# Performance work log

Hardware: AMD Instinct MI355X
Metric: run time of the kernel (lower is better)

Reference implementation:

```python
import jax, jax.numpy as jnp
import numpy as np
import math

B, S, H, NH = 8, 1024, 768, 12
DH = H // NH  # 64
EPS = 1e-5


def layernorm(x, gamma, beta):
    mu = jnp.mean(x, axis=-1, keepdims=True)
    var = jnp.mean(jnp.square(x - mu), axis=-1, keepdims=True)
    return (x - mu) * jax.lax.rsqrt(var + EPS) * gamma + beta


def setup_inputs() -> dict:
    key = jax.random.key(0)
    ks = jax.random.split(key, 12)
    sc = 1.0 / math.sqrt(H)
    return {
        "x1": jax.random.normal(ks[0], (B, S, H), jnp.float32),
        "weight_mask": jax.random.uniform(ks[1], (B, 1, S, S), jnp.float32),
        "Wq": jax.random.normal(ks[2], (H, H), jnp.float32) * sc,
        "bq": jnp.zeros((H,), jnp.float32),
        "Wk": jax.random.normal(ks[3], (H, H), jnp.float32) * sc,
        "bk": jnp.zeros((H,), jnp.float32),
        "Wv": jax.random.normal(ks[4], (H, H), jnp.float32) * sc,
        "bv": jnp.zeros((H,), jnp.float32),
        "g1": jnp.ones((H,), jnp.float32),
        "be1": jnp.zeros((H,), jnp.float32),
        "g2": jnp.ones((H,), jnp.float32),
        "be2": jnp.zeros((H,), jnp.float32),
        "W1": jax.random.normal(ks[5], (H, 2 * H), jnp.float32) * sc,
        "b1": jnp.zeros((2 * H,), jnp.float32),
        "W2": jax.random.normal(ks[6], (2 * H, H), jnp.float32) * (1.0 / math.sqrt(2 * H)),
        "b2": jnp.zeros((H,), jnp.float32),
    }


def reference(x1, weight_mask, Wq, bq, Wk, bk, Wv, bv, g1, be1, g2, be2, W1, b1, W2, b2):
    # QKV projections [B,S,H]
    q_mixed = x1 @ Wq + bq
    k_mixed = x1 @ Wk + bk
    v_mixed = x1 @ Wv + bv

    def heads(t):  # [B,S,H] -> [B,NH,S,DH]
        return t.reshape(B, S, NH, DH).transpose(0, 2, 1, 3)

    q, k, v = heads(q_mixed), heads(k_mixed), heads(v_mixed)
    scores = jnp.einsum("bhqd,bhkd->bhqk", q, k) / math.sqrt(DH)
    probs = jax.nn.softmax(scores, axis=-1)
    probs = probs * weight_mask  # post-softmax elementwise mask
    ctx = jnp.einsum("bhqk,bhkd->bhqd", probs, v)
    ctx = ctx.transpose(0, 2, 1, 3).reshape(B, S, H)

    # residual uses the mixed query (as in the original code); dropout = eval identity
    x = layernorm(ctx + q_mixed, g1, be1)
    ff = jnp.maximum(x @ W1 + b1, 0.0) @ W2 + b2
    out = layernorm(x + ff, g2, be2)
    return out
```

## Files before the change

kernel.cpp:

```cpp
#include <hip/hip_runtime.h>
#include <math.h>

#define Bsz 8
#define Sq  1024
#define Hd  768
#define NHd 12
#define DHd 64
#define QS  2304

typedef __attribute__((ext_vector_type(8))) short bf16x8;
typedef __attribute__((ext_vector_type(4))) short bf16x4;
typedef __attribute__((ext_vector_type(4))) float f32x4;
typedef __attribute__((ext_vector_type(16))) float f32x16;

__device__ __forceinline__ ushort f2bf(float f) {
    unsigned u = __float_as_uint(f);
    u += 0x7fffu + ((u >> 16) & 1u);
    return (ushort)(u >> 16);
}
__device__ __forceinline__ float bf2f(ushort u) {
    return __uint_as_float(((unsigned)u) << 16);
}
__device__ __forceinline__ void load_lds16(const ushort* g, ushort* l) {
    __builtin_amdgcn_global_load_lds((const __attribute__((address_space(1))) void*)g,
                                     (__attribute__((address_space(3))) void*)l, 16, 0, 0);
}

__device__ __forceinline__ f32x16 mfma32x8(bf16x4 a, bf16x4 b, f32x16 c) {
#if __has_builtin(__builtin_amdgcn_mfma_f32_32x32x8bf16_1k)
    return __builtin_amdgcn_mfma_f32_32x32x8bf16_1k(a, b, c, 0, 0, 0);
#elif __has_builtin(__builtin_amdgcn_mfma_f32_32x32x8_bf16)
    return __builtin_amdgcn_mfma_f32_32x32x8_bf16(a, b, c, 0, 0, 0);
#else
    bf16x8 a8 = {a[0], a[1], a[2], a[3], 0, 0, 0, 0};
    bf16x8 b8 = {b[0], b[1], b[2], b[3], 0, 0, 0, 0};
    return __builtin_amdgcn_mfma_f32_32x32x16_bf16(a8, b8, c, 0, 0, 0);
#endif
}

__global__ __launch_bounds__(256) void cvt_bf16(const float* __restrict__ a,
                                                ushort* __restrict__ o, int n4) {
    int i = blockIdx.x * 256 + threadIdx.x;
    if (i < n4) {
        float4 f = ((const float4*)a)[i];
        ushort4 u;
        u.x = f2bf(f.x); u.y = f2bf(f.y); u.z = f2bf(f.z); u.w = f2bf(f.w);
        ((ushort4*)o)[i] = u;
    }
}

__global__ __launch_bounds__(256) void transpose_cvt(const float* __restrict__ in,
                                                     ushort* __restrict__ out,
                                                     int K, int N, float scale) {
    __shared__ float tile[32][33];
    const int n0 = blockIdx.x * 32, k0 = blockIdx.y * 32;
    const int tx = threadIdx.x & 31, ty = threadIdx.x >> 5;
#pragma unroll
    for (int i = ty; i < 32; i += 8)
        tile[i][tx] = in[(size_t)(k0 + i) * N + n0 + tx] * scale;
    __syncthreads();
#pragma unroll
    for (int i = ty; i < 32; i += 8)
        out[(size_t)(n0 + i) * K + k0 + tx] = f2bf(tile[tx][i]);
}

#define KSCALE 0.18033688f

__global__ __launch_bounds__(256) void concat_bias(const float* __restrict__ bq,
                                                   const float* __restrict__ bk,
                                                   const float* __restrict__ bv,
                                                   float* __restrict__ o) {
    int i = blockIdx.x * 256 + threadIdx.x;
    if (i < 2304)
        o[i] = i < 768 ? bq[i] : (i < 1536 ? bk[i - 768] * KSCALE : bv[i - 1536]);
}

template<bool RELU, bool OUT_BF16>
__global__ __launch_bounds__(256) void gemm_mfma(const ushort* __restrict__ A,
                                                 const ushort* __restrict__ BT,
                                                 const float* __restrict__ bias,
                                                 void* __restrict__ Cout,
                                                 int M, int N, int K) {
    const int bm = blockIdx.y * 128;
    const int bn = blockIdx.x * 128;
    const int t  = threadIdx.x;
    const int wave = t >> 6, lane = t & 63;
    const int l15 = lane & 15, quad = lane >> 4;
    const int wm = (wave >> 1) * 64, wn = (wave & 1) * 64;

    __shared__ ushort As[128 * 64];
    __shared__ ushort Bs[128 * 64];

    f32x4 acc[4][4];
#pragma unroll
    for (int i = 0; i < 4; ++i)
#pragma unroll
        for (int j = 0; j < 4; ++j) acc[i][j] = (f32x4){0, 0, 0, 0};

    const int g_row[4] = {(0 * 256 + t) >> 3, (1 * 256 + t) >> 3, (2 * 256 + t) >> 3, (3 * 256 + t) >> 3};
    const int g_pc     = t & 7;

    for (int k0 = 0; k0 < K; k0 += 64) {
#pragma unroll
        for (int it = 0; it < 4; ++it) {
            const int row = g_row[it];
            const int cb  = g_pc ^ (row & 7);
            load_lds16(A  + (size_t)(bm + row) * K + k0 + cb * 8,
                       As + (size_t)(it * 256 + wave * 64) * 8);
            load_lds16(BT + (size_t)(bn + row) * K + k0 + cb * 8,
                       Bs + (size_t)(it * 256 + wave * 64) * 8);
        }
        __syncthreads();
#pragma unroll
        for (int kk = 0; kk < 64; kk += 32) {
            bf16x8 af[4], bfr[4];
            const int cbk = (kk >> 3) + quad;
#pragma unroll
            for (int i = 0; i < 4; ++i) {
                const int rowA = wm + i * 16 + l15;
                af[i]  = *(const bf16x8*)(As + (size_t)(rowA * 8 + (cbk ^ (rowA & 7))) * 8);
                const int rowB = wn + i * 16 + l15;
                bfr[i] = *(const bf16x8*)(Bs + (size_t)(rowB * 8 + (cbk ^ (rowB & 7))) * 8);
            }
#pragma unroll
            for (int i = 0; i < 4; ++i)
#pragma unroll
                for (int j = 0; j < 4; ++j)
                    acc[i][j] = __builtin_amdgcn_mfma_f32_16x16x32_bf16(af[i], bfr[j], acc[i][j], 0, 0, 0);
        }
        __syncthreads();
    }

#pragma unroll
    for (int i = 0; i < 4; ++i) {
#pragma unroll
        for (int r = 0; r < 4; ++r) {
            const int m = bm + wm + i * 16 + quad * 4 + r;
#pragma unroll
            for (int j = 0; j < 4; ++j) {
                const int n = bn + wn + j * 16 + l15;
                float v = acc[i][j][r] + bias[n];
                if (RELU) v = fmaxf(v, 0.0f);
                if (OUT_BF16) ((ushort*)Cout)[(size_t)m * N + n] = f2bf(v);
                else          ((float*)Cout)[(size_t)m * N + n] = v;
            }
        }
    }
}

__global__ __launch_bounds__(256) void v_transpose(const ushort* __restrict__ qkv,
                                                   ushort* __restrict__ vT) {
    const int bh = blockIdx.x >> 4;
    const int st = blockIdx.x & 15;
    const int b  = bh / NHd, h = bh % NHd;
    const int t  = threadIdx.x;
    __shared__ ushort T[64][72];
    {
        const int sl = t >> 2, c = (t & 3) * 16;
        const ushort* src = qkv + ((size_t)b * Sq + st * 64 + sl) * QS + 1536 + h * 64 + c;
        *(int4*)&T[sl][c]     = *(const int4*)src;
        *(int4*)&T[sl][c + 8] = *(const int4*)(src + 8);
    }
    __syncthreads();
    {
        const int d = t >> 2, kc = (t & 3) * 16;
        ushort tmp[16];
#pragma unroll
        for (int i = 0; i < 16; ++i) tmp[i] = T[kc + i][d];
        ushort* dst = vT + ((size_t)bh * 64 + d) * Sq + st * 64 + kc;
        *(int4*)dst       = *(const int4*)&tmp[0];
        *(int4*)(dst + 8) = *(const int4*)&tmp[8];
    }
}

__global__ __launch_bounds__(256, 3) void attn_mfma(const ushort* __restrict__ qkv,
                                                    const ushort* __restrict__ vT,
                                                    const ushort* __restrict__ maskb,
                                                    float* __restrict__ ctx) {
    const int nqt = Sq / 128;
    const int bh  = blockIdx.x / nqt;
    const int qt  = blockIdx.x % nqt;
    const int b   = bh / NHd;
    const int h   = bh % NHd;
    const int t   = threadIdx.x;
    const int wave = t >> 6, lane = t & 63;
    const int l31 = lane & 31, H = lane >> 5;

    __shared__ ushort Ks[2][64 * 64];
    __shared__ ushort Vs[2][64 * 64];

    const size_t rowbase = (size_t)b * Sq;
    const int q0 = qt * 128 + wave * 32;

    bf16x8 qf[4];
    {
        const ushort* qrow = qkv + (rowbase + q0 + l31) * QS + h * DHd + H * 8;
#pragma unroll
        for (int ds = 0; ds < 4; ++ds) qf[ds] = *(const bf16x8*)(qrow + ds * 16);
    }

    const int s_row[2] = {t >> 3, (256 + t) >> 3};
    const int s_pc     = t & 7;

#define STAGE(k0_, buf_)                                                            \
    {                                                                               \
        _Pragma("unroll")                                                           \
        for (int it = 0; it < 2; ++it) {                                            \
            const int row  = s_row[it];                                             \
            const int gcol = s_pc ^ (row & 7);                                      \
            load_lds16(qkv + (rowbase + (k0_) + row) * QS + Hd + h * DHd + gcol * 8,\
                       &Ks[buf_][(it * 256 + t) * 8]);                              \
            load_lds16(vT + ((size_t)bh * 64 + row) * Sq + (k0_) + gcol * 8,        \
                       &Vs[buf_][(it * 256 + t) * 8]);                              \
        }                                                                           \
    }

    STAGE(0, 0);
    __syncthreads();

    f32x16 o0, o1;
#pragma unroll
    for (int r = 0; r < 16; ++r) { o0[r] = 0.0f; o1[r] = 0.0f; }
    float rsum = 0.0f;

    const ushort* mrow = maskb + ((size_t)b * Sq + q0 + l31) * Sq;

    for (int kt = 0; kt < 16; ++kt) {
        const int k0  = kt * 64;
        const int cur = kt & 1;

        if (kt < 15) STAGE(k0 + 64, cur ^ 1);

        ushort4 mload[8];
#pragma unroll
        for (int tile = 0; tile < 2; ++tile)
#pragma unroll
            for (int rr = 0; rr < 4; ++rr)
                mload[tile * 4 + rr] = *(const ushort4*)(mrow + k0 + tile * 32 + rr * 8 + H * 4);

        f32x16 s0, s1;
#pragma unroll
        for (int r = 0; r < 16; ++r) { s0[r] = 0.0f; s1[r] = 0.0f; }
#pragma unroll
        for (int ds = 0; ds < 4; ++ds) {
            const int gk = H + 2 * ds;
            bf16x8 ka = *(const bf16x8*)&Ks[cur][(l31 * 8 + (gk ^ (l31 & 7))) * 8];
            bf16x8 kb = *(const bf16x8*)&Ks[cur][((32 + l31) * 8 + (gk ^ (l31 & 7))) * 8];
            s0 = __builtin_amdgcn_mfma_f32_32x32x16_bf16(ka, qf[ds], s0, 0, 0, 0);
            s1 = __builtin_amdgcn_mfma_f32_32x32x16_bf16(kb, qf[ds], s1, 0, 0, 0);
        }

        bf16x4 pf[8];
#pragma unroll
        for (int rr = 0; rr < 4; ++rr) {
#pragma unroll
            for (int j = 0; j < 4; ++j) {
                const float e0 = exp2f(s0[4 * rr + j]);
                const float e1 = exp2f(s1[4 * rr + j]);
                rsum += e0 + e1;
                pf[rr][j]     = (short)f2bf(e0 * bf2f(((const ushort*)&mload[rr])[j]));
                pf[4 + rr][j] = (short)f2bf(e1 * bf2f(((const ushort*)&mload[4 + rr])[j]));
            }
        }

#pragma unroll
        for (int ks = 0; ks < 8; ++ks) {
            const int sw = ks ^ (l31 & 7);
            bf16x4 va = *(const bf16x4*)&Vs[cur][(l31 * 8 + sw) * 8 + H * 4];
            bf16x4 vb = *(const bf16x4*)&Vs[cur][((32 + l31) * 8 + sw) * 8 + H * 4];
            o0 = mfma32x8(pf[ks], va, o0);
            o1 = mfma32x8(pf[ks], vb, o1);
        }
        __syncthreads();
    }

    rsum += __shfl_xor(rsum, 32);

#pragma unroll
    for (int r = 0; r < 16; ++r) {
        const int ql  = (r & 3) + 8 * (r >> 2) + 4 * H;
        const float inv = 1.0f / __shfl(rsum, ql);
        const size_t row = rowbase + q0 + ql;
        ctx[row * Hd + h * DHd + l31]      = o0[r] * inv;
        ctx[row * Hd + h * DHd + 32 + l31] = o1[r] * inv;
    }
}

template<bool RES_BF16, bool EMIT_BF16>
__global__ __launch_bounds__(256) void ln_fused(const float* __restrict__ a,
                                                const void* __restrict__ res, int res_stride,
                                                const float* __restrict__ g,
                                                const float* __restrict__ be,
                                                float* __restrict__ outf,
                                                ushort* __restrict__ outb) {
    const int row = blockIdx.x;
    const int t   = threadIdx.x;
    const float* pa = a + (size_t)row * Hd;
    __shared__ float red[4];
    float v[3];
#pragma unroll
    for (int i = 0; i < 3; ++i) {
        const int idx = t + i * 256;
        float rv;
        if (RES_BF16) rv = bf2f(((const ushort*)res)[(size_t)row * res_stride + idx]);
        else          rv = ((const float*)res)[(size_t)row * res_stride + idx];
        v[i] = pa[idx] + rv;
    }

    float s = v[0] + v[1] + v[2];
#pragma unroll
    for (int off = 32; off > 0; off >>= 1) s += __shfl_xor(s, off);
    if ((t & 63) == 0) red[t >> 6] = s;
    __syncthreads();
    const float mu = (red[0] + red[1] + red[2] + red[3]) * (1.0f / Hd);
    __syncthreads();

    float sq = 0.0f;
#pragma unroll
    for (int i = 0; i < 3; ++i) {
        v[i] -= mu;
        sq = fmaf(v[i], v[i], sq);
    }
#pragma unroll
    for (int off = 32; off > 0; off >>= 1) sq += __shfl_xor(sq, off);
    if ((t & 63) == 0) red[t >> 6] = sq;
    __syncthreads();
    const float var = (red[0] + red[1] + red[2] + red[3]) * (1.0f / Hd);
    const float rsq = rsqrtf(var + 1e-5f);
#pragma unroll
    for (int i = 0; i < 3; ++i) {
        const int idx = t + i * 256;
        const float o = v[i] * rsq * g[idx] + be[idx];
        outf[(size_t)row * Hd + idx] = o;
        if (EMIT_BF16) outb[(size_t)row * Hd + idx] = f2bf(o);
    }
}

extern "C" void kernel_launch(void* const* d_in, const int* in_sizes, int n_in,
                              void* d_out, int out_size, void* d_ws, size_t ws_size,
                              hipStream_t stream) {
    const float* x1    = (const float*)d_in[0];
    const float* wmask = (const float*)d_in[1];
    const float* Wq    = (const float*)d_in[2];
    const float* bq    = (const float*)d_in[3];
    const float* Wk    = (const float*)d_in[4];
    const float* bk    = (const float*)d_in[5];
    const float* Wv    = (const float*)d_in[6];
    const float* bv    = (const float*)d_in[7];
    const float* g1    = (const float*)d_in[8];
    const float* be1   = (const float*)d_in[9];
    const float* g2    = (const float*)d_in[10];
    const float* be2   = (const float*)d_in[11];
    const float* W1    = (const float*)d_in[12];
    const float* b1    = (const float*)d_in[13];
    const float* W2    = (const float*)d_in[14];
    const float* b2    = (const float*)d_in[15];
    float* out = (float*)d_out;

    const size_t NT = (size_t)Bsz * Sq * Hd;
    const size_t NM = (size_t)Bsz * Sq * Sq;
    const int M = Bsz * Sq;

    char* p = (char*)d_ws;
    ushort* xb     = (ushort*)p;  p += NT * 2;
    ushort* WqkvT  = (ushort*)p;  p += (size_t)2304 * 768 * 2;
    ushort* W1T    = (ushort*)p;  p += (size_t)1536 * 768 * 2;
    ushort* W2T    = (ushort*)p;  p += (size_t)768 * 1536 * 2;
    float*  qkvbias= (float*)p;   p += 2304 * 4 + 256;
    ushort* qkvb   = (ushort*)p;  p += (size_t)M * QS * 2;
    ushort* maskb  = (ushort*)p;  p += NM * 2;
    ushort* vT     = (ushort*)p;  p += (size_t)Bsz * NHd * DHd * Sq * 2;
    float*  ctxb   = (float*)p;   p += NT * 4;
    float*  xf     = (float*)p;   p += NT * 4;
    ushort* xbf    = (ushort*)p;  p += NT * 2;
    ushort* hb     = qkvb;
    float*  ffb    = ctxb;

    dim3 blk(256);

    cvt_bf16<<<dim3((int)(NT / 4 / 256)), blk, 0, stream>>>(x1, xb, (int)(NT / 4));
    cvt_bf16<<<dim3((int)(NM / 4 / 256)), blk, 0, stream>>>(wmask, maskb, (int)(NM / 4));

    transpose_cvt<<<dim3(24, 24), blk, 0, stream>>>(Wq, WqkvT,                 768, 768, 1.0f);
    transpose_cvt<<<dim3(24, 24), blk, 0, stream>>>(Wk, WqkvT + 768 * 768,     768, 768, KSCALE);
    transpose_cvt<<<dim3(24, 24), blk, 0, stream>>>(Wv, WqkvT + 2 * 768 * 768, 768, 768, 1.0f);
    transpose_cvt<<<dim3(48, 24), blk, 0, stream>>>(W1, W1T, 768, 1536, 1.0f);
    transpose_cvt<<<dim3(24, 48), blk, 0, stream>>>(W2, W2T, 1536, 768, 1.0f);
    concat_bias<<<dim3(9), blk, 0, stream>>>(bq, bk, bv, qkvbias);

    gemm_mfma<false, true><<<dim3(2304 / 128, M / 128), blk, 0, stream>>>(
        xb, WqkvT, qkvbias, qkvb, M, 2304, 768);

    v_transpose<<<dim3(Bsz * NHd * 16), blk, 0, stream>>>(qkvb, vT);

    attn_mfma<<<dim3(Bsz * NHd * (Sq / 128)), blk, 0, stream>>>(qkvb, vT, maskb, ctxb);

    ln_fused<true, true><<<dim3(M), blk, 0, stream>>>(ctxb, qkvb, QS, g1, be1, xf, xbf);

    gemm_mfma<true, true><<<dim3(1536 / 128, M / 128), blk, 0, stream>>>(
        xbf, W1T, b1, hb, M, 1536, 768);

    gemm_mfma<false, false><<<dim3(768 / 128, M / 128), blk, 0, stream>>>(
        hb, W2T, b2, ffb, M, 768, 1536);

    ln_fused<false, false><<<dim3(M), blk, 0, stream>>>(xf, ffb, Hd, g2, be2, out, nullptr);
}
```

Baseline: 384.9 us.

## Merge prep kernels, fuse V transpose into QKV GEMM, shrink W2 GEMM tile

Nine separate conversion, transpose and bias-concat launches become one multi-role prep kernel. The standalone V transpose kernel is removed: the QKV GEMM now writes the V columns straight into the transposed vT layout as packed ushort4 stores. The GEMM is templated on its M tile, and the W2 GEMM uses 64-row tiles to launch more blocks. The attention probability conversion now truncates to bf16 instead of rounding, which trades a little accuracy for fewer instructions.

```diff
diff --git a/kernel.cpp b/kernel.cpp
--- a/kernel.cpp
+++ b/kernel.cpp
@@ -38,92 +38,126 @@
 #endif
 }
 
-__global__ __launch_bounds__(256) void cvt_bf16(const float* __restrict__ a,
-                                                ushort* __restrict__ o, int n4) {
-    int i = blockIdx.x * 256 + threadIdx.x;
-    if (i < n4) {
-        float4 f = ((const float4*)a)[i];
-        ushort4 u;
-        u.x = f2bf(f.x); u.y = f2bf(f.y); u.z = f2bf(f.z); u.w = f2bf(f.w);
-        ((ushort4*)o)[i] = u;
-    }
-}
-
-__global__ __launch_bounds__(256) void transpose_cvt(const float* __restrict__ in,
-                                                     ushort* __restrict__ out,
-                                                     int K, int N, float scale) {
-    __shared__ float tile[32][33];
-    const int n0 = blockIdx.x * 32, k0 = blockIdx.y * 32;
-    const int tx = threadIdx.x & 31, ty = threadIdx.x >> 5;
-#pragma unroll
-    for (int i = ty; i < 32; i += 8)
-        tile[i][tx] = in[(size_t)(k0 + i) * N + n0 + tx] * scale;
-    __syncthreads();
-#pragma unroll
-    for (int i = ty; i < 32; i += 8)
-        out[(size_t)(n0 + i) * K + k0 + tx] = f2bf(tile[tx][i]);
-}
-
 #define KSCALE 0.18033688f
 
-__global__ __launch_bounds__(256) void concat_bias(const float* __restrict__ bq,
-                                                   const float* __restrict__ bk,
-                                                   const float* __restrict__ bv,
-                                                   float* __restrict__ o) {
-    int i = blockIdx.x * 256 + threadIdx.x;
-    if (i < 2304)
-        o[i] = i < 768 ? bq[i] : (i < 1536 ? bk[i - 768] * KSCALE : bv[i - 1536]);
-}
-
-template<bool RELU, bool OUT_BF16>
+__global__ __launch_bounds__(256) void prep(const float* __restrict__ x1,
+                                            const float* __restrict__ wmask,
+                                            const float* __restrict__ Wq,
+                                            const float* __restrict__ Wk,
+                                            const float* __restrict__ Wv,
+                                            const float* __restrict__ W1,
+                                            const float* __restrict__ W2,
+                                            const float* __restrict__ bq,
+                                            const float* __restrict__ bk,
+                                            const float* __restrict__ bv,
+                                            ushort* __restrict__ xb,
+                                            ushort* __restrict__ maskb,
+                                            ushort* __restrict__ WqkvT,
+                                            ushort* __restrict__ W1T,
+                                            ushort* __restrict__ W2T,
+                                            float* __restrict__ qkvbias) {
+    const int blk = blockIdx.x;
+    const int t   = threadIdx.x;
+    __shared__ float tl[32][33];
+
+    if (blk < 4032) {
+        const float* in; ushort* out; int Kd, Nd, ntx, tile; float sc;
+        if (blk < 1728) {
+            const int w = blk / 576; tile = blk % 576;
+            in  = (w == 0) ? Wq : (w == 1) ? Wk : Wv;
+            out = WqkvT + (size_t)w * 768 * 768;
+            Kd = 768; Nd = 768; ntx = 24;
+            sc = (w == 1) ? KSCALE : 1.0f;
+        } else if (blk < 2880) {
+            tile = blk - 1728; in = W1; out = W1T; Kd = 768; Nd = 1536; ntx = 48; sc = 1.0f;
+        } else {
+            tile = blk - 2880; in = W2; out = W2T; Kd = 1536; Nd = 768; ntx = 24; sc = 1.0f;
+        }
+        const int n0 = (tile % ntx) * 32, k0 = (tile / ntx) * 32;
+        const int tx = t & 31, ty = t >> 5;
+#pragma unroll
+        for (int i = ty; i < 32; i += 8)
+            tl[i][tx] = in[(size_t)(k0 + i) * Nd + n0 + tx] * sc;
+        __syncthreads();
+#pragma unroll
+        for (int i = ty; i < 32; i += 8)
+            out[(size_t)(n0 + i) * Kd + k0 + tx] = f2bf(tl[tx][i]);
+    } else if (blk < 7616) {
+        const int cb = blk - 4032;
+        const float4* s4;
+        ushort4* d4;
+        if (cb < 1536) { s4 = (const float4*)x1    + (size_t)cb * 1024;           d4 = (ushort4*)xb    + (size_t)cb * 1024; }
+        else           { s4 = (const float4*)wmask + (size_t)(cb - 1536) * 1024;  d4 = (ushort4*)maskb + (size_t)(cb - 1536) * 1024; }
+#pragma unroll
+        for (int i = t; i < 1024; i += 256) {
+            const float4 f = s4[i];
+            ushort4 u;
+            u.x = f2bf(f.x); u.y = f2bf(f.y); u.z = f2bf(f.z); u.w = f2bf(f.w);
+            d4[i] = u;
+        }
+    } else {
+        for (int i = t; i < 2304; i += 256)
+            qkvbias[i] = i < 768 ? bq[i] : (i < 1536 ? bk[i - 768] * KSCALE : bv[i - 1536]);
+    }
+}
+
+template<int TM, bool RELU, bool OUT_BF16, bool WRITE_VT>
 __global__ __launch_bounds__(256) void gemm_mfma(const ushort* __restrict__ A,
                                                  const ushort* __restrict__ BT,
                                                  const float* __restrict__ bias,
                                                  void* __restrict__ Cout,
+                                                 ushort* __restrict__ vT,
                                                  int M, int N, int K) {
-    const int bm = blockIdx.y * 128;
+    const int bm = blockIdx.y * (TM * 32);
     const int bn = blockIdx.x * 128;
     const int t  = threadIdx.x;
     const int wave = t >> 6, lane = t & 63;
     const int l15 = lane & 15, quad = lane >> 4;
-    const int wm = (wave >> 1) * 64, wn = (wave & 1) * 64;
-
-    __shared__ ushort As[128 * 64];
+    const int wm = (wave >> 1) * (TM * 16), wn = (wave & 1) * 64;
+
+    __shared__ ushort As[TM * 32 * 64];
     __shared__ ushort Bs[128 * 64];
 
-    f32x4 acc[4][4];
-#pragma unroll
-    for (int i = 0; i < 4; ++i)
+    f32x4 acc[TM][4];
+#pragma unroll
+    for (int i = 0; i < TM; ++i)
 #pragma unroll
         for (int j = 0; j < 4; ++j) acc[i][j] = (f32x4){0, 0, 0, 0};
 
-    const int g_row[4] = {(0 * 256 + t) >> 3, (1 * 256 + t) >> 3, (2 * 256 + t) >> 3, (3 * 256 + t) >> 3};
-    const int g_pc     = t & 7;
+    const int g_pc = t & 7;
 
     for (int k0 = 0; k0 < K; k0 += 64) {
 #pragma unroll
+        for (int it = 0; it < TM; ++it) {
+            const int row = (it * 256 + t) >> 3;
+            const int cb  = g_pc ^ (row & 7);
+            load_lds16(A + (size_t)(bm + row) * K + k0 + cb * 8,
+                       As + (size_t)(it * 256 + wave * 64) * 8);
+        }
+#pragma unroll
         for (int it = 0; it < 4; ++it) {
-            const int row = g_row[it];
+            const int row = (it * 256 + t) >> 3;
             const int cb  = g_pc ^ (row & 7);
-            load_lds16(A  + (size_t)(bm + row) * K + k0 + cb * 8,
-                       As + (size_t)(it * 256 + wave * 64) * 8);
             load_lds16(BT + (size_t)(bn + row) * K + k0 + cb * 8,
                        Bs + (size_t)(it * 256 + wave * 64) * 8);
         }
         __syncthreads();
 #pragma unroll
         for (int kk = 0; kk < 64; kk += 32) {
-            bf16x8 af[4], bfr[4];
+            bf16x8 af[TM], bfr[4];
             const int cbk = (kk >> 3) + quad;
 #pragma unroll
-            for (int i = 0; i < 4; ++i) {
+            for (int i = 0; i < TM; ++i) {
                 const int rowA = wm + i * 16 + l15;
-                af[i]  = *(const bf16x8*)(As + (size_t)(rowA * 8 + (cbk ^ (rowA & 7))) * 8);
-                const int rowB = wn + i * 16 + l15;
-                bfr[i] = *(const bf16x8*)(Bs + (size_t)(rowB * 8 + (cbk ^ (rowB & 7))) * 8);
+                af[i] = *(const bf16x8*)(As + (size_t)(rowA * 8 + (cbk ^ (rowA & 7))) * 8);
             }
 #pragma unroll
-            for (int i = 0; i < 4; ++i)
+            for (int j = 0; j < 4; ++j) {
+                const int rowB = wn + j * 16 + l15;
+                bfr[j] = *(const bf16x8*)(Bs + (size_t)(rowB * 8 + (cbk ^ (rowB & 7))) * 8);
+            }
+#pragma unroll
+            for (int i = 0; i < TM; ++i)
 #pragma unroll
                 for (int j = 0; j < 4; ++j)
                     acc[i][j] = __builtin_amdgcn_mfma_f32_16x16x32_bf16(af[i], bfr[j], acc[i][j], 0, 0, 0);
@@ -131,45 +165,34 @@
         __syncthreads();
     }
 
-#pragma unroll
-    for (int i = 0; i < 4; ++i) {
-#pragma unroll
-        for (int r = 0; r < 4; ++r) {
-            const int m = bm + wm + i * 16 + quad * 4 + r;
-#pragma unroll
-            for (int j = 0; j < 4; ++j) {
-                const int n = bn + wn + j * 16 + l15;
+    const bool vblk = WRITE_VT && (bn >= 1536);
+#pragma unroll
+    for (int i = 0; i < TM; ++i) {
+        const int m0 = bm + wm + i * 16 + quad * 4;
+#pragma unroll
+        for (int j = 0; j < 4; ++j) {
+            const int n = bn + wn + j * 16 + l15;
+            float v4[4];
+#pragma unroll
+            for (int r = 0; r < 4; ++r) {
                 float v = acc[i][j][r] + bias[n];
                 if (RELU) v = fmaxf(v, 0.0f);
-                if (OUT_BF16) ((ushort*)Cout)[(size_t)m * N + n] = f2bf(v);
-                else          ((float*)Cout)[(size_t)m * N + n] = v;
+                v4[r] = v;
             }
-        }
-    }
-}
-
-__global__ __launch_bounds__(256) void v_transpose(const ushort* __restrict__ qkv,
-                                                   ushort* __restrict__ vT) {
-    const int bh = blockIdx.x >> 4;
-    const int st = blockIdx.x & 15;
-    const int b  = bh / NHd, h = bh % NHd;
-    const int t  = threadIdx.x;
-    __shared__ ushort T[64][72];
-    {
-        const int sl = t >> 2, c = (t & 3) * 16;
-        const ushort* src = qkv + ((size_t)b * Sq + st * 64 + sl) * QS + 1536 + h * 64 + c;
-        *(int4*)&T[sl][c]     = *(const int4*)src;
-        *(int4*)&T[sl][c + 8] = *(const int4*)(src + 8);
-    }
-    __syncthreads();
-    {
-        const int d = t >> 2, kc = (t & 3) * 16;
-        ushort tmp[16];
-#pragma unroll
-        for (int i = 0; i < 16; ++i) tmp[i] = T[kc + i][d];
-        ushort* dst = vT + ((size_t)bh * 64 + d) * Sq + st * 64 + kc;
-        *(int4*)dst       = *(const int4*)&tmp[0];
-        *(int4*)(dst + 8) = *(const int4*)&tmp[8];
+            if (vblk) {
+                const int d = n - 1536;
+                const int b = m0 >> 10, s = m0 & 1023;
+                ushort4 pk;
+                pk.x = f2bf(v4[0]); pk.y = f2bf(v4[1]); pk.z = f2bf(v4[2]); pk.w = f2bf(v4[3]);
+                *(ushort4*)(vT + ((size_t)(b * NHd + (d >> 6)) * 64 + (d & 63)) * Sq + s) = pk;
+            } else {
+#pragma unroll
+                for (int r = 0; r < 4; ++r) {
+                    if (OUT_BF16) ((ushort*)Cout)[(size_t)(m0 + r) * N + n] = f2bf(v4[r]);
+                    else          ((float*)Cout)[(size_t)(m0 + r) * N + n] = v4[r];
+                }
+            }
+        }
     }
 }
 
@@ -258,8 +281,8 @@
                 const float e0 = exp2f(s0[4 * rr + j]);
                 const float e1 = exp2f(s1[4 * rr + j]);
                 rsum += e0 + e1;
-                pf[rr][j]     = (short)f2bf(e0 * bf2f(((const ushort*)&mload[rr])[j]));
-                pf[4 + rr][j] = (short)f2bf(e1 * bf2f(((const ushort*)&mload[4 + rr])[j]));
+                pf[rr][j]     = (short)(__float_as_uint(e0 * bf2f(((const ushort*)&mload[rr])[j])) >> 16);
+                pf[4 + rr][j] = (short)(__float_as_uint(e1 * bf2f(((const ushort*)&mload[4 + rr])[j])) >> 16);
             }
         }
 
@@ -378,30 +401,21 @@
 
     dim3 blk(256);
 
-    cvt_bf16<<<dim3((int)(NT / 4 / 256)), blk, 0, stream>>>(x1, xb, (int)(NT / 4));
-    cvt_bf16<<<dim3((int)(NM / 4 / 256)), blk, 0, stream>>>(wmask, maskb, (int)(NM / 4));
-
-    transpose_cvt<<<dim3(24, 24), blk, 0, stream>>>(Wq, WqkvT,                 768, 768, 1.0f);
-    transpose_cvt<<<dim3(24, 24), blk, 0, stream>>>(Wk, WqkvT + 768 * 768,     768, 768, KSCALE);
-    transpose_cvt<<<dim3(24, 24), blk, 0, stream>>>(Wv, WqkvT + 2 * 768 * 768, 768, 768, 1.0f);
-    transpose_cvt<<<dim3(48, 24), blk, 0, stream>>>(W1, W1T, 768, 1536, 1.0f);
-    transpose_cvt<<<dim3(24, 48), blk, 0, stream>>>(W2, W2T, 1536, 768, 1.0f);
-    concat_bias<<<dim3(9), blk, 0, stream>>>(bq, bk, bv, qkvbias);
-
-    gemm_mfma<false, true><<<dim3(2304 / 128, M / 128), blk, 0, stream>>>(
-        xb, WqkvT, qkvbias, qkvb, M, 2304, 768);
-
-    v_transpose<<<dim3(Bsz * NHd * 16), blk, 0, stream>>>(qkvb, vT);
+    prep<<<dim3(7617), blk, 0, stream>>>(x1, wmask, Wq, Wk, Wv, W1, W2, bq, bk, bv,
+                                         xb, maskb, WqkvT, W1T, W2T, qkvbias);
+
+    gemm_mfma<4, false, true, true><<<dim3(2304 / 128, M / 128), blk, 0, stream>>>(
+        xb, WqkvT, qkvbias, qkvb, vT, M, 2304, 768);
 
     attn_mfma<<<dim3(Bsz * NHd * (Sq / 128)), blk, 0, stream>>>(qkvb, vT, maskb, ctxb);
 
     ln_fused<true, true><<<dim3(M), blk, 0, stream>>>(ctxb, qkvb, QS, g1, be1, xf, xbf);
 
-    gemm_mfma<true, true><<<dim3(1536 / 128, M / 128), blk, 0, stream>>>(
-        xbf, W1T, b1, hb, M, 1536, 768);
-
-    gemm_mfma<false, false><<<dim3(768 / 128, M / 128), blk, 0, stream>>>(
-        hb, W2T, b2, ffb, M, 768, 1536);
+    gemm_mfma<4, true, true, false><<<dim3(1536 / 128, M / 128), blk, 0, stream>>>(
+        xbf, W1T, b1, hb, nullptr, M, 1536, 768);
+
+    gemm_mfma<2, false, false, false><<<dim3(768 / 128, M / 64), blk, 0, stream>>>(
+        hb, W2T, b2, ffb, nullptr, M, 768, 1536);
 
     ln_fused<false, false><<<dim3(M), blk, 0, stream>>>(xf, ffb, Hd, g2, be2, out, nullptr);
 }
```

Result: faster. 358.4 us (-6.9%).
